# Kernel tuning notes

Measured on AMD Instinct MI355X. Metric: run time of the kernel, lower is better.

The kernel has to match this reference:

```python
import math
import jax, jax.numpy as jnp
import numpy as np

NEG_INF_FILL = 1e-09  # faithful to the source: masked positions get +1e-09, not -inf

B, H, S, D = 2, 16, 2048, 64


def setup_inputs() -> dict:
    key = jax.random.key(0)
    kq, kk, kv = jax.random.split(key, 3)
    q = jax.random.normal(kq, (B, H, S, D), dtype=jnp.float32)
    k = jax.random.normal(kk, (B, H, S, D), dtype=jnp.float32)
    v = jax.random.normal(kv, (B, H, S, D), dtype=jnp.float32)
    # causal boolean mask, broadcast over heads: [B, 1, S, S]
    causal = jnp.tril(jnp.ones((S, S), dtype=bool))
    attention_mask = jnp.broadcast_to(causal[None, None, :, :], (B, 1, S, S))
    return {"q": q, "k": k, "v": v, "attention_mask": attention_mask}


def reference(q, k, v, attention_mask):
    d_k = q.shape[-1]
    # scores: [B, H, S, S]
    scores = jnp.einsum("bhqd,bhkd->bhqk", q, k) / math.sqrt(d_k)
    scores = jnp.where(attention_mask, scores, NEG_INF_FILL)
    attn = jax.nn.softmax(scores, axis=-1)
    # output: [B, H, S, D]
    return jnp.einsum("bhqk,bhkd->bhqd", attn, v)
```

## Files before the change

kernel.cpp:

```cpp
#include <hip/hip_runtime.h>
#include <hip/hip_bf16.h>


#define SEQ 2048
#define DIM 64
#define NEG_FILL 1e-9f
#define KS_STRIDE 72
#define PS_STRIDE 72

typedef _Float16 half_t;
typedef _Float16 half8  __attribute__((ext_vector_type(8)));
typedef _Float16 half4v __attribute__((ext_vector_type(4)));
typedef _Float16 half2v __attribute__((ext_vector_type(2)));
typedef float    float4v __attribute__((ext_vector_type(4)));

__global__ __launch_bounds__(256)
void vchunk_kernel(const float* __restrict__ V, float* __restrict__ part) {
    __shared__ float red[16][68];
    const int bh = blockIdx.x, ch = blockIdx.y;
    const int t = threadIdx.x;
    const float* Vc = V + ((size_t)bh * SEQ + ch * 128) * DIM;
    float s0 = 0.f, s1 = 0.f, s2 = 0.f, s3 = 0.f;
    #pragma unroll
    for (int i = 0; i < 8; ++i) {
        float4v x = *(const float4v*)(Vc + 4 * (t + 256 * i));
        s0 += x[0]; s1 += x[1]; s2 += x[2]; s3 += x[3];
    }
    const int dg = t & 15, rg = t >> 4;
    red[rg][4 * dg + 0] = s0; red[rg][4 * dg + 1] = s1;
    red[rg][4 * dg + 2] = s2; red[rg][4 * dg + 3] = s3;
    __syncthreads();
    if (t < 64) {
        float s = 0.f;
        #pragma unroll
        for (int r = 0; r < 16; ++r) s += red[r][t];
        part[((size_t)bh * 16 + ch) * 64 + t] = s;
    }
}

__global__ __launch_bounds__(256, 2)
void attn_mfma_kernel(const float* __restrict__ Q,
                      const float* __restrict__ K,
                      const float* __restrict__ V,
                      const float* __restrict__ part,
                      float* __restrict__ O) {
    __shared__ half_t smem_h[64 * KS_STRIDE + 64 * KS_STRIDE + 4 * 32 * PS_STRIDE];
    half_t* Ks  = smem_h;
    half_t* VTs = smem_h + 64 * KS_STRIDE;
    half_t* Ps  = smem_h + 2 * 64 * KS_STRIDE;

    const int tid = threadIdx.x;
    const int l   = tid & 63;
    const int w   = tid >> 6;
    const int lx  = l & 15;
    const int h   = l >> 4;
    const int bh  = blockIdx.x;
    const int qb  = 15 - (int)blockIdx.y;
    const int qbase = qb * 128;
    const int nkt = 2 * qb + 2;
    const int n_tail = SEQ - nkt * 64;

    const float* Qh = Q + (size_t)bh * SEQ * DIM;
    const float* Kh = K + (size_t)bh * SEQ * DIM;
    const float* Vh = V + (size_t)bh * SEQ * DIM;
    float*       Oh = O + (size_t)bh * SEQ * DIM;

    half8 qf[2][2];
    const int qrow_w = qbase + 32 * w;
    #pragma unroll
    for (int nt = 0; nt < 2; ++nt) {
        const float* qp = Qh + (size_t)(qrow_w + 16 * nt + lx) * DIM;
        #pragma unroll
        for (int s = 0; s < 2; ++s) {
            float4v a = *(const float4v*)(qp + 32 * s + 8 * h);
            float4v b = *(const float4v*)(qp + 32 * s + 8 * h + 4);
            half8 f;
            f[0] = (half_t)(a[0] * 0.125f); f[1] = (half_t)(a[1] * 0.125f);
            f[2] = (half_t)(a[2] * 0.125f); f[3] = (half_t)(a[3] * 0.125f);
            f[4] = (half_t)(b[0] * 0.125f); f[5] = (half_t)(b[1] * 0.125f);
            f[6] = (half_t)(b[2] * 0.125f); f[7] = (half_t)(b[3] * 0.125f);
            qf[nt][s] = f;
        }
    }

    float4v acc[4][2];
    #pragma unroll
    for (int mt = 0; mt < 4; ++mt)
        #pragma unroll
        for (int nt = 0; nt < 2; ++nt) acc[mt][nt] = (float4v){0.f, 0.f, 0.f, 0.f};
    float lp[2] = {0.f, 0.f};

    const int c = tid & 15;
    const int r0 = tid >> 4;

    float4v kreg[4], vreg[4];
    {
        const float* Kt = Kh;
        const float* Vt = Vh;
        #pragma unroll
        for (int u = 0; u < 4; ++u)
            kreg[u] = *(const float4v*)(Kt + (r0 + 16 * u) * DIM + 4 * c);
        #pragma unroll
        for (int u = 0; u < 2; ++u) {
            const float* vp = Vt + (size_t)(2 * (r0 + 16 * u)) * DIM + 4 * c;
            vreg[2 * u]     = *(const float4v*)(vp);
            vreg[2 * u + 1] = *(const float4v*)(vp + DIM);
        }
    }

    for (int kt = 0; kt < nkt; ++kt) {
        __syncthreads();

        #pragma unroll
        for (int u = 0; u < 4; ++u) {
            int kr = r0 + 16 * u;
            half4v hk;
            hk[0] = (half_t)kreg[u][0]; hk[1] = (half_t)kreg[u][1];
            hk[2] = (half_t)kreg[u][2]; hk[3] = (half_t)kreg[u][3];
            *(half4v*)(Ks + kr * KS_STRIDE + 4 * c) = hk;
        }
        #pragma unroll
        for (int u = 0; u < 2; ++u) {
            int kp = r0 + 16 * u;
            #pragma unroll
            for (int i = 0; i < 4; ++i) {
                int ir = (i + c + (c >> 2)) & 3;
                int dr = 4 * c + ir;
                half2v hv;
                hv[0] = (half_t)vreg[2 * u][ir];
                hv[1] = (half_t)vreg[2 * u + 1][ir];
                *(half2v*)(VTs + dr * KS_STRIDE + 2 * kp) = hv;
            }
        }
        __syncthreads();

        if (kt + 1 < nkt) {
            const float* Kt = Kh + (size_t)(kt + 1) * 64 * DIM;
            const float* Vt = Vh + (size_t)(kt + 1) * 64 * DIM;
            #pragma unroll
            for (int u = 0; u < 4; ++u)
                kreg[u] = *(const float4v*)(Kt + (r0 + 16 * u) * DIM + 4 * c);
            #pragma unroll
            for (int u = 0; u < 2; ++u) {
                const float* vp = Vt + (size_t)(2 * (r0 + 16 * u)) * DIM + 4 * c;
                vreg[2 * u]     = *(const float4v*)(vp);
                vreg[2 * u + 1] = *(const float4v*)(vp + DIM);
            }
        }

        const int key_base = kt * 64;
        #pragma unroll
        for (int mt = 0; mt < 4; ++mt) {
            half8 ak0 = *(const half8*)(Ks + (16 * mt + lx) * KS_STRIDE + 8 * h);
            half8 ak1 = *(const half8*)(Ks + (16 * mt + lx) * KS_STRIDE + 32 + 8 * h);
            #pragma unroll
            for (int nt = 0; nt < 2; ++nt) {
                float4v ct = (float4v){0.f, 0.f, 0.f, 0.f};
                ct = __builtin_amdgcn_mfma_f32_16x16x32_f16(ak0, qf[nt][0], ct, 0, 0, 0);
                ct = __builtin_amdgcn_mfma_f32_16x16x32_f16(ak1, qf[nt][1], ct, 0, 0, 0);
                const int qg = qrow_w + 16 * nt + lx;
                const int kb = key_base + 16 * mt + 4 * h;
                float p[4];
                #pragma unroll
                for (int r = 0; r < 4; ++r) {
                    float sv = ct[r];
                    if (kb + r > qg) sv = NEG_FILL;
                    p[r] = __expf(sv);
                }
                lp[nt] += (p[0] + p[1]) + (p[2] + p[3]);
                half4v hp;
                hp[0] = (half_t)p[0]; hp[1] = (half_t)p[1];
                hp[2] = (half_t)p[2]; hp[3] = (half_t)p[3];
                *(half4v*)(Ps + w * (32 * PS_STRIDE) + (16 * nt + lx) * PS_STRIDE
                           + 16 * mt + 4 * h) = hp;
            }
        }

        half8 pf[2][2];
        #pragma unroll
        for (int nt = 0; nt < 2; ++nt)
            #pragma unroll
            for (int s = 0; s < 2; ++s)
                pf[nt][s] = *(const half8*)(Ps + w * (32 * PS_STRIDE)
                                            + (16 * nt + lx) * PS_STRIDE + 32 * s + 8 * h);
        #pragma unroll
        for (int mt = 0; mt < 4; ++mt) {
            half8 av0 = *(const half8*)(VTs + (16 * mt + lx) * KS_STRIDE + 8 * h);
            half8 av1 = *(const half8*)(VTs + (16 * mt + lx) * KS_STRIDE + 32 + 8 * h);
            #pragma unroll
            for (int nt = 0; nt < 2; ++nt) {
                float4v ct = acc[mt][nt];
                ct = __builtin_amdgcn_mfma_f32_16x16x32_f16(av0, pf[nt][0], ct, 0, 0, 0);
                ct = __builtin_amdgcn_mfma_f32_16x16x32_f16(av1, pf[nt][1], ct, 0, 0, 0);
                acc[mt][nt] = ct;
            }
        }
    }

    float linv[2];
    #pragma unroll
    for (int nt = 0; nt < 2; ++nt) {
        float s = lp[nt];
        s += __shfl_xor(s, 16, 64);
        s += __shfl_xor(s, 32, 64);
        linv[nt] = 1.0f / (s + (float)n_tail);
    }

    float* vtf = ((float*)smem_h) + 8320;
    __syncthreads();
    if (tid < 64) {
        float s = 0.f;
        for (int ch = qb + 1; ch < 16; ++ch)
            s += part[((size_t)bh * 16 + ch) * 64 + tid];
        vtf[tid] = s;
    }
    __syncthreads();
    float vt_l[4][4];
    #pragma unroll
    for (int mt = 0; mt < 4; ++mt)
        #pragma unroll
        for (int r = 0; r < 4; ++r) vt_l[mt][r] = vtf[16 * mt + 4 * h + r];

    float* Osm = (float*)smem_h;
    #pragma unroll
    for (int mt = 0; mt < 4; ++mt)
        #pragma unroll
        for (int nt = 0; nt < 2; ++nt)
            #pragma unroll
            for (int r = 0; r < 4; ++r) {
                float o = (acc[mt][nt][r] + vt_l[mt][r]) * linv[nt];
                Osm[w * (32 * 65) + (16 * nt + lx) * 65 + 16 * mt + 4 * h + r] = o;
            }
    __syncthreads();
    #pragma unroll
    for (int u = 0; u < 8; ++u) {
        int row = r0 + 16 * u;
        int dc = 4 * c;
        const float* src = Osm + (row >> 5) * (32 * 65) + (row & 31) * 65 + dc;
        float4v ov = {src[0], src[1], src[2], src[3]};
        *(float4v*)(Oh + (size_t)(qbase + row) * DIM + dc) = ov;
    }
}

extern "C" void kernel_launch(void* const* d_in, const int* in_sizes, int n_in,
                              void* d_out, int out_size, void* d_ws, size_t ws_size,
                              hipStream_t stream) {
    const float* q = (const float*)d_in[0];
    const float* k = (const float*)d_in[1];
    const float* v = (const float*)d_in[2];
    float* out = (float*)d_out;
    float* part = (float*)d_ws;

    vchunk_kernel<<<dim3(32, 16), 256, 0, stream>>>(v, part);
    attn_mfma_kernel<<<dim3(32, 16), 256, 0, stream>>>(q, k, v, part, out);
}
```

Baseline: 156.0 us.

## Fuse V tail-sum into attention kernel, use exp2 and skip mask on interior tiles

Drops the separate V chunk-sum kernel and its launch. Each attention block now sums the fully masked tail rows of V itself, reduces them through shared memory, and no longer reads the workspace buffer. Q is prescaled by log2(e)/8 so the exponential is a bare exp2, and the causal mask compare runs only on tiles that cross the diagonal; masked entries are set to 1, which is exp(1e-9) in fp32. The cost is that blocks with few key tiles now re-read long V tails redundantly inside the main kernel, which adds load imbalance.

```diff
diff --git a/kernel.cpp b/kernel.cpp
--- a/kernel.cpp
+++ b/kernel.cpp
@@ -4,9 +4,9 @@
 
 #define SEQ 2048
 #define DIM 64
-#define NEG_FILL 1e-9f
 #define KS_STRIDE 72
 #define PS_STRIDE 72
+#define QSCALE 0.18033688011112042f
 
 typedef _Float16 half_t;
 typedef _Float16 half8  __attribute__((ext_vector_type(8)));
@@ -14,35 +14,10 @@
 typedef _Float16 half2v __attribute__((ext_vector_type(2)));
 typedef float    float4v __attribute__((ext_vector_type(4)));
 
-__global__ __launch_bounds__(256)
-void vchunk_kernel(const float* __restrict__ V, float* __restrict__ part) {
-    __shared__ float red[16][68];
-    const int bh = blockIdx.x, ch = blockIdx.y;
-    const int t = threadIdx.x;
-    const float* Vc = V + ((size_t)bh * SEQ + ch * 128) * DIM;
-    float s0 = 0.f, s1 = 0.f, s2 = 0.f, s3 = 0.f;
-    #pragma unroll
-    for (int i = 0; i < 8; ++i) {
-        float4v x = *(const float4v*)(Vc + 4 * (t + 256 * i));
-        s0 += x[0]; s1 += x[1]; s2 += x[2]; s3 += x[3];
-    }
-    const int dg = t & 15, rg = t >> 4;
-    red[rg][4 * dg + 0] = s0; red[rg][4 * dg + 1] = s1;
-    red[rg][4 * dg + 2] = s2; red[rg][4 * dg + 3] = s3;
-    __syncthreads();
-    if (t < 64) {
-        float s = 0.f;
-        #pragma unroll
-        for (int r = 0; r < 16; ++r) s += red[r][t];
-        part[((size_t)bh * 16 + ch) * 64 + t] = s;
-    }
-}
-
 __global__ __launch_bounds__(256, 2)
 void attn_mfma_kernel(const float* __restrict__ Q,
                       const float* __restrict__ K,
                       const float* __restrict__ V,
-                      const float* __restrict__ part,
                       float* __restrict__ O) {
     __shared__ half_t smem_h[64 * KS_STRIDE + 64 * KS_STRIDE + 4 * 32 * PS_STRIDE];
     half_t* Ks  = smem_h;
@@ -75,10 +50,10 @@
             float4v a = *(const float4v*)(qp + 32 * s + 8 * h);
             float4v b = *(const float4v*)(qp + 32 * s + 8 * h + 4);
             half8 f;
-            f[0] = (half_t)(a[0] * 0.125f); f[1] = (half_t)(a[1] * 0.125f);
-            f[2] = (half_t)(a[2] * 0.125f); f[3] = (half_t)(a[3] * 0.125f);
-            f[4] = (half_t)(b[0] * 0.125f); f[5] = (half_t)(b[1] * 0.125f);
-            f[6] = (half_t)(b[2] * 0.125f); f[7] = (half_t)(b[3] * 0.125f);
+            f[0] = (half_t)(a[0] * QSCALE); f[1] = (half_t)(a[1] * QSCALE);
+            f[2] = (half_t)(a[2] * QSCALE); f[3] = (half_t)(a[3] * QSCALE);
+            f[4] = (half_t)(b[0] * QSCALE); f[5] = (half_t)(b[1] * QSCALE);
+            f[6] = (half_t)(b[2] * QSCALE); f[7] = (half_t)(b[3] * QSCALE);
             qf[nt][s] = f;
         }
     }
@@ -95,14 +70,12 @@
 
     float4v kreg[4], vreg[4];
     {
-        const float* Kt = Kh;
-        const float* Vt = Vh;
         #pragma unroll
         for (int u = 0; u < 4; ++u)
-            kreg[u] = *(const float4v*)(Kt + (r0 + 16 * u) * DIM + 4 * c);
+            kreg[u] = *(const float4v*)(Kh + (r0 + 16 * u) * DIM + 4 * c);
         #pragma unroll
         for (int u = 0; u < 2; ++u) {
-            const float* vp = Vt + (size_t)(2 * (r0 + 16 * u)) * DIM + 4 * c;
+            const float* vp = Vh + (size_t)(2 * (r0 + 16 * u)) * DIM + 4 * c;
             vreg[2 * u]     = *(const float4v*)(vp);
             vreg[2 * u + 1] = *(const float4v*)(vp + DIM);
         }
@@ -153,19 +126,22 @@
         for (int mt = 0; mt < 4; ++mt) {
             half8 ak0 = *(const half8*)(Ks + (16 * mt + lx) * KS_STRIDE + 8 * h);
             half8 ak1 = *(const half8*)(Ks + (16 * mt + lx) * KS_STRIDE + 32 + 8 * h);
+            const bool need_mask = (key_base + 16 * mt + 15) > qrow_w;
             #pragma unroll
             for (int nt = 0; nt < 2; ++nt) {
                 float4v ct = (float4v){0.f, 0.f, 0.f, 0.f};
                 ct = __builtin_amdgcn_mfma_f32_16x16x32_f16(ak0, qf[nt][0], ct, 0, 0, 0);
                 ct = __builtin_amdgcn_mfma_f32_16x16x32_f16(ak1, qf[nt][1], ct, 0, 0, 0);
-                const int qg = qrow_w + 16 * nt + lx;
-                const int kb = key_base + 16 * mt + 4 * h;
                 float p[4];
                 #pragma unroll
-                for (int r = 0; r < 4; ++r) {
-                    float sv = ct[r];
-                    if (kb + r > qg) sv = NEG_FILL;
-                    p[r] = __expf(sv);
+                for (int r = 0; r < 4; ++r)
+                    p[r] = __builtin_amdgcn_exp2f(ct[r]);
+                if (need_mask) {
+                    const int qg = qrow_w + 16 * nt + lx;
+                    const int kb = key_base + 16 * mt + 4 * h;
+                    #pragma unroll
+                    for (int r = 0; r < 4; ++r)
+                        if (kb + r > qg) p[r] = 1.0f;
                 }
                 lp[nt] += (p[0] + p[1]) + (p[2] + p[3]);
                 half4v hp;
@@ -206,12 +182,29 @@
         linv[nt] = 1.0f / (s + (float)n_tail);
     }
 
-    float* vtf = ((float*)smem_h) + 8320;
+    float ts0 = 0.f, ts1 = 0.f, ts2 = 0.f, ts3 = 0.f;
+    {
+        const int tstart = nkt * 64;
+        const float* vp = Vh + (size_t)tstart * DIM + 4 * c;
+        #pragma unroll 4
+        for (int k = tstart + r0; k < SEQ; k += 16) {
+            float4v x = *(const float4v*)(Vh + (size_t)k * DIM + 4 * c);
+            ts0 += x[0]; ts1 += x[1]; ts2 += x[2]; ts3 += x[3];
+        }
+        (void)vp;
+    }
+    __syncthreads();
+    float* preS = (float*)smem_h;
+    float* vtf  = ((float*)smem_h) + 8320;
+    {
+        float4v pv = {ts0, ts1, ts2, ts3};
+        *(float4v*)(preS + r0 * 68 + 4 * c) = pv;
+    }
     __syncthreads();
     if (tid < 64) {
         float s = 0.f;
-        for (int ch = qb + 1; ch < 16; ++ch)
-            s += part[((size_t)bh * 16 + ch) * 64 + tid];
+        #pragma unroll
+        for (int p = 0; p < 16; ++p) s += preS[p * 68 + tid];
         vtf[tid] = s;
     }
     __syncthreads();
@@ -249,8 +242,5 @@
     const float* k = (const float*)d_in[1];
     const float* v = (const float*)d_in[2];
     float* out = (float*)d_out;
-    float* part = (float*)d_ws;
-
-    vchunk_kernel<<<dim3(32, 16), 256, 0, stream>>>(v, part);
-    attn_mfma_kernel<<<dim3(32, 16), 256, 0, stream>>>(q, k, v, part, out);
+    attn_mfma_kernel<<<dim3(32, 16), 256, 0, stream>>>(q, k, v, out);
 }
```

Result: faster. 148.7 us (-4.7%).
